# Kernel tuning notes

Hardware: AMD Instinct MI355X
Metric: run time of the kernel (lower is better)

## Reference

```python
import jax, jax.numpy as jnp
import numpy as np

ALPHA = 0.2  # LeakyReLU negative slope
NEG_BIG = -9e15


def setup_inputs() -> dict:
    key = jax.random.key(0)
    k1, k2, k3, k4 = jax.random.split(key, 4)
    B, N, F_in, F_out = 8, 2048, 256, 256
    x = jax.random.normal(k1, (B, N, F_in), dtype=jnp.float32)
    adj = jax.random.randint(k2, (B, N, N), 0, 2, dtype=jnp.int32)
    # Xavier-uniform init like nn.init.xavier_uniform_
    limW = float(np.sqrt(6.0 / (F_in + F_out)))
    W = jax.random.uniform(k3, (F_in, F_out), minval=-limW, maxval=limW, dtype=jnp.float32)
    lima = float(np.sqrt(6.0 / (2 * F_out + 1)))
    a = jax.random.uniform(k4, (2 * F_out, 1), minval=-lima, maxval=lima, dtype=jnp.float32)
    return {"x": x, "adj": adj, "W": W, "a": a}


def reference(x, adj, W, a):
    # x: (B,N,Fin), adj: (B,N,N), W: (Fin,Fout), a: (2*Fout,1)
    F_out = W.shape[1]
    Wh = jnp.einsum('bnf,fo->bno', x, W)            # (B,N,Fout)
    a1, a2 = a[:F_out, 0], a[F_out:, 0]
    # e[b,i,j] = leakyrelu(Wh[b,i]@a1 + Wh[b,j]@a2)  (equivalent to concat+matmul)
    e = (Wh @ a1)[:, :, None] + (Wh @ a2)[:, None, :]  # (B,N,N)
    e = jnp.where(e > 0, e, ALPHA * e)
    attention = jnp.where(adj > 0, e, NEG_BIG)
    attention = jax.nn.softmax(attention, axis=-1)
    # dropout is identity in eval mode (training=False)
    h_prime = jnp.einsum('bij,bjo->bio', attention, Wh)  # (B,N,Fout)
    return jax.nn.elu(h_prime)  # concat=True -> ELU
```

## Files before the change

kernel.cpp:

```cpp
#include <hip/hip_runtime.h>
#include <hip/hip_fp16.h>

typedef _Float16 f16;
typedef _Float16 half4 __attribute__((ext_vector_type(4)));
typedef _Float16 half8 __attribute__((ext_vector_type(8)));
typedef float f32x4 __attribute__((ext_vector_type(4)));

#define BATCH 8
#define NTOK 2048
#define FIN 256
#define FOUT 256
#define ALPHA 0.2f


__device__ __forceinline__ void gload16(const void* g, void* l) {
    __builtin_amdgcn_global_load_lds(
        (const __attribute__((address_space(1))) unsigned int*)(g),
        (__attribute__((address_space(3))) unsigned int*)(l), 16, 0, 0);
}

__global__ void k_wt(const float* __restrict__ W, f16* __restrict__ WT) {
    __shared__ float t[32][33];
    int o0 = blockIdx.x * 32, k0 = blockIdx.y * 32;
    int tx = threadIdx.x, ty = threadIdx.y;
    t[ty][tx] = W[(k0 + ty) * FOUT + o0 + tx];
    __syncthreads();
    WT[(o0 + ty) * FIN + (k0 + tx)] = (f16)t[tx][ty];
}

__global__ __launch_bounds__(256) void k_pack(const int* __restrict__ adj,
                                              unsigned long long* __restrict__ mask) {
    int lane = threadIdx.x & 63;
    size_t wv = (((size_t)blockIdx.x * 256 + threadIdx.x) >> 6);
    for (int it = 0; it < 8; it++) {
        size_t wave = wv + (size_t)it * 16384;
        const int* base = adj + wave * 256;
        unsigned long long m0 = __ballot(base[lane] > 0);
        unsigned long long m1 = __ballot(base[64 + lane] > 0);
        unsigned long long m2 = __ballot(base[128 + lane] > 0);
        unsigned long long m3 = __ballot(base[192 + lane] > 0);
        if (lane < 4) {
            unsigned long long v = lane == 0 ? m0 : lane == 1 ? m1 : lane == 2 ? m2 : m3;
            mask[wave * 4 + lane] = v;
        }
    }
}

__global__ __launch_bounds__(256) void k_gemm(const float* __restrict__ x,
                                              const f16* __restrict__ WT,
                                              const float* __restrict__ a,
                                              f16* __restrict__ WhT,
                                              float* __restrict__ s1,
                                              float* __restrict__ s2) {
    __shared__ __align__(16) char gsmem[46080];
    int t = threadIdx.x;
    f16* Ah = (f16*)gsmem;
    f16* Bt = (f16*)(gsmem + 9216);
    int m0 = blockIdx.x * 64;
    int lane = t & 63, w = t >> 6;
    int lr = lane & 15, lg = lane >> 4;
    f32x4 acc[4][4] = {};

    for (int k0 = 0; k0 < FIN; k0 += 64) {
        {
            int r = t >> 2, c = (t & 3) * 16;
            const float* src = x + (size_t)(m0 + r) * FIN + k0 + c;
            f32x4 v0 = *(const f32x4*)(src);
            f32x4 v1 = *(const f32x4*)(src + 4);
            f32x4 v2 = *(const f32x4*)(src + 8);
            f32x4 v3 = *(const f32x4*)(src + 12);
            half8 h0, h1;
#pragma unroll
            for (int q = 0; q < 4; q++) {
                h0[q] = (f16)v0[q]; h0[q + 4] = (f16)v1[q];
                h1[q] = (f16)v2[q]; h1[q + 4] = (f16)v3[q];
            }
            f16* dst = Ah + r * 72 + c;
            *(half8*)dst = h0;
            *(half8*)(dst + 8) = h1;
        }
        {
            const f16* src = WT + (size_t)t * FIN + k0;
            f16* dst = Bt + t * 72;
#pragma unroll
            for (int q = 0; q < 8; q++)
                *(half8*)(dst + q * 8) = *(const half8*)(src + q * 8);
        }
        __syncthreads();
#pragma unroll
        for (int kc = 0; kc < 2; kc++) {
            int krow = kc * 32 + lg * 8;
            half8 af[4], bf[4];
#pragma unroll
            for (int fi = 0; fi < 4; fi++)
                af[fi] = *(half8*)(Ah + (fi * 16 + lr) * 72 + krow);
#pragma unroll
            for (int fo = 0; fo < 4; fo++)
                bf[fo] = *(half8*)(Bt + (w * 64 + fo * 16 + lr) * 72 + krow);
#pragma unroll
            for (int fi = 0; fi < 4; fi++)
#pragma unroll
                for (int fo = 0; fo < 4; fo++)
                    acc[fi][fo] = __builtin_amdgcn_mfma_f32_16x16x32_f16(
                        af[fi], bf[fo], acc[fi][fo], 0, 0, 0);
        }
        __syncthreads();
    }

    int b = m0 >> 11;
    int slab_i = (m0 & (NTOK - 1)) >> 6;
    int nbase = m0 & (NTOK - 1);

    float* sred = (float*)gsmem;
    f16* slab = (f16*)(gsmem + 9216);
    float a1v[4], a2v[4];
#pragma unroll
    for (int fo = 0; fo < 4; fo++) {
        int o = w * 64 + fo * 16 + lr;
        a1v[fo] = a[o];
        a2v[fo] = a[FOUT + o];
    }
#pragma unroll
    for (int fi = 0; fi < 4; fi++) {
        f32x4 p1 = {}, p2 = {};
#pragma unroll
        for (int fo = 0; fo < 4; fo++) {
            p1 += acc[fi][fo] * a1v[fo];
            p2 += acc[fi][fo] * a2v[fo];
        }
#pragma unroll
        for (int q = 0; q < 4; q++) {
#pragma unroll
            for (int d = 1; d < 16; d <<= 1) {
                p1[q] += __shfl_xor(p1[q], d);
                p2[q] += __shfl_xor(p2[q], d);
            }
        }
        if (lr == 0) {
            int row = fi * 16 + lg * 4;
#pragma unroll
            for (int q = 0; q < 4; q++) {
                sred[w * 64 + row + q] = p1[q];
                sred[256 + w * 64 + row + q] = p2[q];
            }
        }
    }
#pragma unroll
    for (int fi = 0; fi < 4; fi++) {
        int jg8 = fi * 2 + (lg >> 1), jq0 = (lg & 1) * 4;
#pragma unroll
        for (int fo = 0; fo < 4; fo++) {
            int o = w * 64 + fo * 16 + lr;
            half4 hv;
#pragma unroll
            for (int q = 0; q < 4; q++) hv[q] = (f16)acc[fi][fo][q];
            *(half4*)(slab + o * 64 + ((jg8 ^ (o & 7)) * 8) + jq0) = hv;
        }
    }
    __syncthreads();

    if (t < 64) {
        s1[(size_t)b * NTOK + nbase + t] =
            sred[t] + sred[64 + t] + sred[128 + t] + sred[192 + t];
    } else if (t < 128) {
        int r2 = t - 64;
        s2[(size_t)b * NTOK + nbase + r2] =
            sred[256 + r2] + sred[320 + r2] + sred[384 + r2] + sred[448 + r2];
    }
    {
        const int4* sl = (const int4*)slab;
        int4* gd = (int4*)(WhT + ((size_t)(b * 32 + slab_i) * 256) * 64);
#pragma unroll
        for (int i = 0; i < 8; i++) gd[i * 256 + t] = sl[i * 256 + t];
    }
}

__global__ __launch_bounds__(256) void k_rowmax(const float* __restrict__ s1,
                                                const float* __restrict__ s2,
                                                float* __restrict__ mrow) {
    __shared__ float red[4];
    int b = blockIdx.x, t = threadIdx.x;
    const float* s2b = s2 + (size_t)b * NTOK;
    float mx = -3.0e38f;
#pragma unroll
    for (int i = 0; i < 8; i++) mx = fmaxf(mx, s2b[t + i * 256]);
#pragma unroll
    for (int d = 1; d < 64; d <<= 1) mx = fmaxf(mx, __shfl_xor(mx, d));
    if ((t & 63) == 0) red[t >> 6] = mx;
    __syncthreads();
    float s2m = fmaxf(fmaxf(red[0], red[1]), fmaxf(red[2], red[3]));
#pragma unroll
    for (int i = 0; i < 8; i++) {
        int n = t + i * 256;
        float s = s1[(size_t)b * NTOK + n] + s2m;
        mrow[(size_t)b * NTOK + n] = fmaxf(s, ALPHA * s);
    }
}

__global__ __launch_bounds__(512, 2) void k_attn(const unsigned* __restrict__ mask32,
                                                 const f16* __restrict__ WhT,
                                                 const float* __restrict__ s1g,
                                                 const float* __restrict__ s2g,
                                                 const float* __restrict__ mg,
                                                 float* __restrict__ out) {
    __shared__ __align__(16) char smem[65536 + 8192 + 512];
    f16* Bl = (f16*)smem;
    float* s2_lds = (float*)(smem + 65536);
    float* lpart = (float*)(smem + 65536 + 8192);

    int b = blockIdx.x & 7;
    int i0 = (blockIdx.x >> 3) * 64;
    int t = threadIdx.x;
    int lane = t & 63, w = t >> 6;
    int js = w & 1, oh = (w >> 1) & 1, rg = w >> 2;
    int lr = lane & 15, lg = lane >> 4;

    ((f32x4*)s2_lds)[t] = ((const f32x4*)(s2g + (size_t)b * NTOK))[t];

    const char* wsrc = (const char*)WhT + (size_t)b * (32 * 32768);
    {
        const char* src = wsrc + (w * 4) * 1024 + lane * 16;
        char* dst = (char*)Bl + (w * 4) * 1024;
#pragma unroll
        for (int k = 0; k < 4; k++) gload16(src + k * 1024, dst + k * 1024);
    }

    int r0 = i0 + rg * 32 + lr, r1 = r0 + 16;
    float s1r0 = s1g[(size_t)b * NTOK + r0];
    float s1r1 = s1g[(size_t)b * NTOK + r1];
    float mx0 = mg[(size_t)b * NTOK + r0];
    float mx1 = mg[(size_t)b * NTOK + r1];
    const unsigned* mr0 = mask32 + (size_t)(b * NTOK + r0) * 64 + js;
    const unsigned* mr1 = mask32 + (size_t)(b * NTOK + r1) * 64 + js;

    f32x4 acc0[8] = {}, acc1[8] = {};
    float l0 = 0.f, l1 = 0.f;
    int rswz = ((js * 4 + lg) ^ (lr & 7)) * 8;

    unsigned bw0 = mr0[0], bw1 = mr1[0];

    __syncthreads();

    for (int s = 0; s < 32; s++) {
        int buf = s & 1;
        if (s < 31) {
            const char* src = wsrc + (size_t)(s + 1) * 32768 + (w * 4) * 1024 + lane * 16;
            char* dst = (char*)Bl + (buf ^ 1) * 32768 + (w * 4) * 1024;
#pragma unroll
            for (int k = 0; k < 4; k++) gload16(src + k * 1024, dst + k * 1024);
        }

        unsigned cw0 = bw0, cw1 = bw1;
        if (s < 31) { bw0 = mr0[(s + 1) * 2]; bw1 = mr1[(s + 1) * 2]; }
        unsigned bits0 = (cw0 >> (lg * 8)) & 0xffu;
        unsigned bits1 = (cw1 >> (lg * 8)) & 0xffu;

        int sb = s * 64 + js * 32 + lg * 8;
        f32x4 sA = *(const f32x4*)&s2_lds[sb];
        f32x4 sB = *(const f32x4*)&s2_lds[sb + 4];

        half8 ph0, ph1;
#pragma unroll
        for (int q = 0; q < 8; q++) {
            float sv = q < 4 ? sA[q & 3] : sB[q & 3];
            float sx = s1r0 + sv;
            float ev = fmaxf(sx, ALPHA * sx);
            float p = ((bits0 >> q) & 1) ? __expf(ev - mx0) : 0.f;
            l0 += p; ph0[q] = (f16)p;
            float sy = s1r1 + sv;
            float eu = fmaxf(sy, ALPHA * sy);
            float u = ((bits1 >> q) & 1) ? __expf(eu - mx1) : 0.f;
            l1 += u; ph1[q] = (f16)u;
        }

        const f16* bbase = Bl + buf * 16384 + (oh * 128 + lr) * 64 + rswz;
#pragma unroll
        for (int ot = 0; ot < 8; ot++) {
            half8 bf = *(const half8*)(bbase + ot * (16 * 64));
            acc0[ot] = __builtin_amdgcn_mfma_f32_16x16x32_f16(ph0, bf, acc0[ot], 0, 0, 0);
            acc1[ot] = __builtin_amdgcn_mfma_f32_16x16x32_f16(ph1, bf, acc1[ot], 0, 0, 0);
        }
        __syncthreads();
    }

    l0 += __shfl_xor(l0, 16); l0 += __shfl_xor(l0, 32);
    l1 += __shfl_xor(l1, 16); l1 += __shfl_xor(l1, 32);
    if (oh == 0 && lg == 0) {
        lpart[js * 64 + rg * 32 + lr] = l0;
        lpart[js * 64 + rg * 32 + 16 + lr] = l1;
    }
    __syncthreads();

    float* accx = (float*)smem;
    if (js == 1) {
#pragma unroll
        for (int ot = 0; ot < 8; ot++)
#pragma unroll
            for (int q = 0; q < 4; q++) {
                accx[(rg * 32 + lg * 4 + q) * 260 + oh * 128 + ot * 16 + lr] = acc0[ot][q];
                accx[(rg * 32 + 16 + lg * 4 + q) * 260 + oh * 128 + ot * 16 + lr] = acc1[ot][q];
            }
    }
    __syncthreads();
    if (js == 0) {
        f32x4 rl0, rl1;
#pragma unroll
        for (int q = 0; q < 4; q++) {
            int ra = rg * 32 + lg * 4 + q, rb = ra + 16;
            rl0[q] = 1.f / (lpart[ra] + lpart[64 + ra]);
            rl1[q] = 1.f / (lpart[rb] + lpart[64 + rb]);
        }
#pragma unroll
        for (int ot = 0; ot < 8; ot++) {
            int o = oh * 128 + ot * 16 + lr;
#pragma unroll
            for (int q = 0; q < 4; q++) {
                int ra = rg * 32 + lg * 4 + q;
                float u = (acc0[ot][q] + accx[ra * 260 + o]) * rl0[q];
                u = u > 0.f ? u : __expf(u) - 1.f;
                __builtin_nontemporal_store(u, &out[((size_t)(b * NTOK + i0 + ra)) * FOUT + o]);
                int rb = ra + 16;
                float v = (acc1[ot][q] + accx[rb * 260 + o]) * rl1[q];
                v = v > 0.f ? v : __expf(v) - 1.f;
                __builtin_nontemporal_store(v, &out[((size_t)(b * NTOK + i0 + rb)) * FOUT + o]);
            }
        }
    }
}

extern "C" void kernel_launch(void* const* d_in, const int* in_sizes, int n_in,
                              void* d_out, int out_size, void* d_ws, size_t ws_size,
                              hipStream_t stream) {
    const float* x = (const float*)d_in[0];
    const int* adj = (const int*)d_in[1];
    const float* W = (const float*)d_in[2];
    const float* a = (const float*)d_in[3];
    float* out = (float*)d_out;

    char* ws = (char*)d_ws;
    f16* WT = (f16*)ws;
    f16* WhT = (f16*)(ws + 131072);
    float* s1 = (float*)(ws + 131072 + 8388608);
    float* s2 = s1 + BATCH * NTOK;
    float* mrow = s2 + BATCH * NTOK;
    unsigned long long* mask64 =
        (unsigned long long*)(ws + 131072 + 8388608 + 196608);

    k_pack<<<dim3(4096), 256, 0, stream>>>(adj, mask64);
    k_wt<<<dim3(FOUT / 32, FIN / 32), dim3(32, 32), 0, stream>>>(W, WT);
    k_gemm<<<dim3(BATCH * NTOK / 64), 256, 0, stream>>>(x, WT, a, WhT, s1, s2);
    k_rowmax<<<dim3(BATCH), 256, 0, stream>>>(s1, s2, mrow);
    k_attn<<<dim3(BATCH * NTOK / 64), 512, 0, stream>>>((const unsigned*)mask64, WhT,
                                                        s1, s2, mrow, out);
}
```

Before: 89.49 us.

## Fuse adjacency mask packing into attention kernel via LDS-staged int loads

Drops the separate k_pack kernel that turned the int32 adjacency into a bitmask. The attention kernel now streams raw adjacency tiles into a double-buffered LDS region with async global-to-LDS loads, overlapped with the WhT tile loads, and tests adj>0 per element. This removes one launch and the bitmask write and read-back. In exchange the attention kernel reads the full int32 adjacency itself and its LDS grows to about 107KB, so launch bounds drop to one block per CU, which lowers occupancy.

```diff
diff --git a/kernel.cpp b/kernel.cpp
--- a/kernel.cpp
+++ b/kernel.cpp
@@ -26,24 +26,6 @@
     t[ty][tx] = W[(k0 + ty) * FOUT + o0 + tx];
     __syncthreads();
     WT[(o0 + ty) * FIN + (k0 + tx)] = (f16)t[tx][ty];
-}
-
-__global__ __launch_bounds__(256) void k_pack(const int* __restrict__ adj,
-                                              unsigned long long* __restrict__ mask) {
-    int lane = threadIdx.x & 63;
-    size_t wv = (((size_t)blockIdx.x * 256 + threadIdx.x) >> 6);
-    for (int it = 0; it < 8; it++) {
-        size_t wave = wv + (size_t)it * 16384;
-        const int* base = adj + wave * 256;
-        unsigned long long m0 = __ballot(base[lane] > 0);
-        unsigned long long m1 = __ballot(base[64 + lane] > 0);
-        unsigned long long m2 = __ballot(base[128 + lane] > 0);
-        unsigned long long m3 = __ballot(base[192 + lane] > 0);
-        if (lane < 4) {
-            unsigned long long v = lane == 0 ? m0 : lane == 1 ? m1 : lane == 2 ? m2 : m3;
-            mask[wave * 4 + lane] = v;
-        }
-    }
 }
 
 __global__ __launch_bounds__(256) void k_gemm(const float* __restrict__ x,
@@ -197,16 +179,17 @@
     }
 }
 
-__global__ __launch_bounds__(512, 2) void k_attn(const unsigned* __restrict__ mask32,
+__global__ __launch_bounds__(512, 1) void k_attn(const int* __restrict__ adj,
                                                  const f16* __restrict__ WhT,
                                                  const float* __restrict__ s1g,
                                                  const float* __restrict__ s2g,
                                                  const float* __restrict__ mg,
                                                  float* __restrict__ out) {
-    __shared__ __align__(16) char smem[65536 + 8192 + 512];
+    __shared__ __align__(16) char smem[65536 + 32768 + 8192 + 512];
     f16* Bl = (f16*)smem;
-    float* s2_lds = (float*)(smem + 65536);
-    float* lpart = (float*)(smem + 65536 + 8192);
+    char* adjL = smem + 65536;
+    float* s2_lds = (float*)(smem + 98304);
+    float* lpart = (float*)(smem + 106496);
 
     int b = blockIdx.x & 7;
     int i0 = (blockIdx.x >> 3) * 64;
@@ -218,11 +201,18 @@
     ((f32x4*)s2_lds)[t] = ((const f32x4*)(s2g + (size_t)b * NTOK))[t];
 
     const char* wsrc = (const char*)WhT + (size_t)b * (32 * 32768);
+    const char* asrc0 = (const char*)adj +
+        ((size_t)(b * NTOK + i0 + (lane >> 1))) * 8192 + w * 32 + (lane & 1) * 16;
+
     {
         const char* src = wsrc + (w * 4) * 1024 + lane * 16;
         char* dst = (char*)Bl + (w * 4) * 1024;
 #pragma unroll
         for (int k = 0; k < 4; k++) gload16(src + k * 1024, dst + k * 1024);
+        char* adst = adjL + w * 2048;
+#pragma unroll
+        for (int k = 0; k < 2; k++)
+            gload16(asrc0 + (size_t)k * 32 * 8192, adst + k * 1024);
     }
 
     int r0 = i0 + rg * 32 + lr, r1 = r0 + 16;
@@ -230,14 +220,12 @@
     float s1r1 = s1g[(size_t)b * NTOK + r1];
     float mx0 = mg[(size_t)b * NTOK + r0];
     float mx1 = mg[(size_t)b * NTOK + r1];
-    const unsigned* mr0 = mask32 + (size_t)(b * NTOK + r0) * 64 + js;
-    const unsigned* mr1 = mask32 + (size_t)(b * NTOK + r1) * 64 + js;
 
     f32x4 acc0[8] = {}, acc1[8] = {};
     float l0 = 0.f, l1 = 0.f;
     int rswz = ((js * 4 + lg) ^ (lr & 7)) * 8;
-
-    unsigned bw0 = mr0[0], bw1 = mr1[0];
+    int achunk = (js * 4 + lg) * 2048;
+    int ar0 = (rg * 32 + lr) * 32, ar1 = ar0 + 512;
 
     __syncthreads();
 
@@ -248,12 +236,20 @@
             char* dst = (char*)Bl + (buf ^ 1) * 32768 + (w * 4) * 1024;
 #pragma unroll
             for (int k = 0; k < 4; k++) gload16(src + k * 1024, dst + k * 1024);
-        }
-
-        unsigned cw0 = bw0, cw1 = bw1;
-        if (s < 31) { bw0 = mr0[(s + 1) * 2]; bw1 = mr1[(s + 1) * 2]; }
-        unsigned bits0 = (cw0 >> (lg * 8)) & 0xffu;
-        unsigned bits1 = (cw1 >> (lg * 8)) & 0xffu;
+            const char* asrc = asrc0 + (s + 1) * 256;
+            char* adst = adjL + (buf ^ 1) * 16384 + w * 2048;
+#pragma unroll
+            for (int k = 0; k < 2; k++)
+                gload16(asrc + (size_t)k * 32 * 8192, adst + k * 1024);
+        }
+
+        const char* ac = adjL + buf * 16384 + achunk;
+        int4 a0 = *(const int4*)(ac + ar0);
+        int4 a0b = *(const int4*)(ac + ar0 + 16);
+        int4 a1 = *(const int4*)(ac + ar1);
+        int4 a1b = *(const int4*)(ac + ar1 + 16);
+        int av0[8] = {a0.x, a0.y, a0.z, a0.w, a0b.x, a0b.y, a0b.z, a0b.w};
+        int av1[8] = {a1.x, a1.y, a1.z, a1.w, a1b.x, a1b.y, a1b.z, a1b.w};
 
         int sb = s * 64 + js * 32 + lg * 8;
         f32x4 sA = *(const f32x4*)&s2_lds[sb];
@@ -265,11 +261,11 @@
             float sv = q < 4 ? sA[q & 3] : sB[q & 3];
             float sx = s1r0 + sv;
             float ev = fmaxf(sx, ALPHA * sx);
-            float p = ((bits0 >> q) & 1) ? __expf(ev - mx0) : 0.f;
+            float p = (av0[q] > 0) ? __expf(ev - mx0) : 0.f;
             l0 += p; ph0[q] = (f16)p;
             float sy = s1r1 + sv;
             float eu = fmaxf(sy, ALPHA * sy);
-            float u = ((bits1 >> q) & 1) ? __expf(eu - mx1) : 0.f;
+            float u = (av1[q] > 0) ? __expf(eu - mx1) : 0.f;
             l1 += u; ph1[q] = (f16)u;
         }
 
@@ -343,13 +339,9 @@
     float* s1 = (float*)(ws + 131072 + 8388608);
     float* s2 = s1 + BATCH * NTOK;
     float* mrow = s2 + BATCH * NTOK;
-    unsigned long long* mask64 =
-        (unsigned long long*)(ws + 131072 + 8388608 + 196608);
-
-    k_pack<<<dim3(4096), 256, 0, stream>>>(adj, mask64);
+
     k_wt<<<dim3(FOUT / 32, FIN / 32), dim3(32, 32), 0, stream>>>(W, WT);
     k_gemm<<<dim3(BATCH * NTOK / 64), 256, 0, stream>>>(x, WT, a, WhT, s1, s2);
     k_rowmax<<<dim3(BATCH), 256, 0, stream>>>(s1, s2, mrow);
-    k_attn<<<dim3(BATCH * NTOK / 64), 512, 0, stream>>>((const unsigned*)mask64, WhT,
-                                                        s1, s2, mrow, out);
-}
+    k_attn<<<dim3(BATCH * NTOK / 64), 512, 0, stream>>>(adj, WhT, s1, s2, mrow, out);
+}
```

After: 81.50 us. 1.1x faster.
